# Kernel tuning notes

Measured on AMD Instinct MI355X. Metric: run time of the kernel, lower is better.

## Reference

```python
import jax, jax.numpy as jnp
import numpy as np

N = 50000        # nodes
E = 800000       # edges (avg degree 16)
IN = 256         # in_feature_dim
H = 4            # heads_num
F = 64           # out_feature_dim per head (H*F == IN)
NEG_SLOPE = 0.2  # LeakyReLU slope used for both scoring and output activation


def setup_inputs() -> dict:
    key = jax.random.key(0)
    ks = jax.random.split(key, 8)
    x = jax.random.normal(ks[0], (N, IN), dtype=jnp.float32)
    edge_src = jax.random.randint(ks[1], (E,), 0, N, dtype=jnp.int32)
    edge_trg = jax.random.randint(ks[2], (E,), 0, N, dtype=jnp.int32)
    # xavier-ish scaled params
    W = jax.random.normal(ks[3], (IN, H * F), dtype=jnp.float32) * 0.06
    a_src = jax.random.normal(ks[4], (H, F), dtype=jnp.float32) * 0.1
    a_trg = jax.random.normal(ks[5], (H, F), dtype=jnp.float32) * 0.1
    skip_w = jax.random.normal(ks[6], (IN, H * F), dtype=jnp.float32) * 0.06
    bias = jnp.zeros((H * F,), dtype=jnp.float32)
    return {"x": x, "W": W, "a_src": a_src, "a_trg": a_trg,
            "skip_w": skip_w, "bias": bias,
            "edge_src": edge_src, "edge_trg": edge_trg}


def _leaky(v):
    return jnp.where(v > 0, v, NEG_SLOPE * v)


def reference(x, W, a_src, a_trg, skip_w, bias, edge_src, edge_trg):
    n_nodes = x.shape[0]
    # node-wise projection: [N, H, F]
    proj = (x @ W).reshape(n_nodes, H, F)
    # per-head attention scores: [N, H]
    s_src = jnp.einsum('nhf,hf->nh', proj, a_src)
    s_trg = jnp.einsum('nhf,hf->nh', proj, a_trg)
    # lift to edges + LeakyReLU scoring: [E, H]
    e = _leaky(s_src[edge_src] + s_trg[edge_trg])
    # neighborhood-aware (scatter) softmax over incoming edges of each target
    e = e - jnp.max(e)                      # global max subtraction, as in the source
    ex = jnp.exp(e)
    denom = jax.ops.segment_sum(ex, edge_trg, num_segments=n_nodes)  # [N, H]
    attn = ex / (denom[edge_trg] + 1e-16)   # [E, H]
    # weighted aggregation: [E, H, F] -> scatter-add -> [N, H, F]
    weighted = proj[edge_src] * attn[..., None]
    out = jax.ops.segment_sum(weighted, edge_trg, num_segments=n_nodes)
    # skip connection (dims differ: in=256 vs per-head 64 -> use skip_proj)
    out = out + (x @ skip_w).reshape(n_nodes, H, F)
    # concat heads + bias + output activation (default LeakyReLU 0.2)
    out = out.reshape(n_nodes, H * F) + bias
    return _leaky(out)
```

## Files before the change

### kernel.cpp

```cpp
#include <hip/hip_runtime.h>
#include <math.h>

constexpr float SLOPE = 0.2f;

typedef __bf16 bf16x8 __attribute__((ext_vector_type(8)));
typedef __bf16 bf16x4 __attribute__((ext_vector_type(4)));
typedef float  f32x4  __attribute__((ext_vector_type(4)));

__device__ __forceinline__ int imin(int a, int b) { return a < b ? a : b; }

__device__ __forceinline__ void glds16(const void* g, void* l) {
    __builtin_amdgcn_global_load_lds(
        (const __attribute__((address_space(1))) unsigned int*)g,
        (__attribute__((address_space(3))) unsigned int*)l,
        16, 0, 0);
}

__global__ __launch_bounds__(256) void prep_k(
    const float* __restrict__ W, const float* __restrict__ skw,
    __bf16* __restrict__ Bt,
    const float* __restrict__ x, __bf16* __restrict__ xb, int nxv, int nxb,
    const int* __restrict__ etrg, int* __restrict__ cnt, int E)
{
    const int b = blockIdx.x;
    if (b < 512) {
        const int i = b * 256 + threadIdx.x;
        const int n = i >> 8, k = i & 255;
        const float v = (n < 256) ? W[k * 256 + n] : skw[k * 256 + (n - 256)];
        Bt[i] = (__bf16)v;
    } else if (b < 512 + nxb) {
        const int gid = (b - 512) * 256 + threadIdx.x;
        if (gid < nxv) {
            const float4 f0 = *(const float4*)(x + (size_t)gid * 8);
            const float4 f1 = *(const float4*)(x + (size_t)gid * 8 + 4);
            bf16x8 v;
            v[0] = (__bf16)f0.x; v[1] = (__bf16)f0.y;
            v[2] = (__bf16)f0.z; v[3] = (__bf16)f0.w;
            v[4] = (__bf16)f1.x; v[5] = (__bf16)f1.y;
            v[6] = (__bf16)f1.z; v[7] = (__bf16)f1.w;
            *(bf16x8*)(xb + (size_t)gid * 8) = v;
        }
    } else {
        const int e = (b - 512 - nxb) * 256 + threadIdx.x;
        if (e < E) atomicAdd(&cnt[etrg[e]], 1);
    }
}

__global__ __launch_bounds__(256, 2) void gemm_mfma(
    const __bf16* __restrict__ xb, const __bf16* __restrict__ Bt,
    __bf16* __restrict__ projb, float* __restrict__ out, int M)
{
    __shared__ __bf16 As[256 * 32];
    __shared__ __bf16 Bs[128 * 32];

    const int t    = threadIdx.x;
    const int w    = t >> 6;
    const int lane = t & 63;
    const int q    = lane >> 4;
    const int ln   = lane & 15;

    const int row0 = blockIdx.x * 256;
    const int bt0  = blockIdx.y * 128;

    f32x4 acc[4][8] = {};

    for (int k0 = 0; k0 < 256; k0 += 32) {
#pragma unroll
        for (int p = 0; p < 4; ++p) {
            const int idx = p * 256 + t;
            const int r   = idx >> 2;
            const int ko  = (idx & 3) * 8;
            const int ga  = imin(row0 + r, M - 1);
            glds16(xb + (size_t)ga * 256 + k0 + ko, &As[idx * 8]);
        }
#pragma unroll
        for (int p = 0; p < 2; ++p) {
            const int idx = p * 256 + t;
            const int r   = idx >> 2;
            const int ko  = (idx & 3) * 8;
            glds16(Bt + (size_t)(bt0 + r) * 256 + k0 + ko, &Bs[idx * 8]);
        }
        asm volatile("s_waitcnt vmcnt(0)" ::: "memory");
        __syncthreads();

        bf16x8 af[4], bfr[8];
#pragma unroll
        for (int rb = 0; rb < 4; ++rb)
            af[rb] = *(const bf16x8*)&As[(w * 64 + rb * 16 + ln) * 32 + q * 8];
#pragma unroll
        for (int cb = 0; cb < 8; ++cb)
            bfr[cb] = *(const bf16x8*)&Bs[(cb * 16 + ln) * 32 + q * 8];
#pragma unroll
        for (int rb = 0; rb < 4; ++rb)
#pragma unroll
            for (int cb = 0; cb < 8; ++cb)
                acc[rb][cb] = __builtin_amdgcn_mfma_f32_16x16x32_bf16(
                    af[rb], bfr[cb], acc[rb][cb], 0, 0, 0);
        __syncthreads();
    }

    const bool isProj  = (blockIdx.y < 2);
    const int  colbase = (blockIdx.y & 1) * 128;
#pragma unroll
    for (int rb = 0; rb < 4; ++rb) {
#pragma unroll
        for (int r = 0; r < 4; ++r) {
            const int grow = row0 + w * 64 + rb * 16 + q * 4 + r;
            if (grow < M) {
#pragma unroll
                for (int cb = 0; cb < 8; ++cb) {
                    const float v = acc[rb][cb][r];
                    const int gcol = colbase + cb * 16 + ln;
                    if (isProj) projb[(size_t)grow * 256 + gcol] = (__bf16)v;
                    else        out[(size_t)grow * 256 + gcol]   = v;
                }
            }
        }
    }
}

__global__ __launch_bounds__(256) void scores_k(
    const __bf16* __restrict__ projb,
    const float* __restrict__ a_src, const float* __restrict__ a_trg,
    float* __restrict__ s_src, float* __restrict__ s_trg, int N)
{
    const int nid  = blockIdx.x * 4 + (threadIdx.x >> 6);
    const int lane = threadIdx.x & 63;
    if (nid >= N) return;

    const bf16x4 p4  = *(const bf16x4*)(projb + (size_t)nid * 256 + lane * 4);
    const float4 as4 = *(const float4*)(a_src + lane * 4);
    const float4 at4 = *(const float4*)(a_trg + lane * 4);

    float vs = (float)p4[0] * as4.x + (float)p4[1] * as4.y +
               (float)p4[2] * as4.z + (float)p4[3] * as4.w;
    float vt = (float)p4[0] * at4.x + (float)p4[1] * at4.y +
               (float)p4[2] * at4.z + (float)p4[3] * at4.w;

#pragma unroll
    for (int d = 8; d > 0; d >>= 1) {
        vs += __shfl_down(vs, d, 16);
        vt += __shfl_down(vt, d, 16);
    }
    if ((lane & 15) == 0) {
        s_src[nid * 4 + (lane >> 4)] = vs;
        s_trg[nid * 4 + (lane >> 4)] = vt;
    }
}

__global__ __launch_bounds__(1024) void scanA(
    const int* __restrict__ cnt, int* __restrict__ off, int* __restrict__ bsum, int N)
{
    __shared__ int wsum[16];
    const int t = threadIdx.x;
    const int lane = t & 63;
    const int w = t >> 6;
    const int i = blockIdx.x * 1024 + t;
    const int v = (i < N) ? cnt[i] : 0;

    int s = v;
#pragma unroll
    for (int d = 1; d < 64; d <<= 1) {
        int o = __shfl_up(s, d);
        if (lane >= d) s += o;
    }
    if (lane == 63) wsum[w] = s;
    __syncthreads();
    if (w == 0 && lane < 16) {
        int ws = wsum[lane];
        int sc = ws;
#pragma unroll
        for (int d = 1; d < 16; d <<= 1) {
            int o = __shfl_up(sc, d);
            if (lane >= d) sc += o;
        }
        wsum[lane] = sc - ws;
    }
    __syncthreads();
    const int excl = wsum[w] + s - v;
    if (i < N) off[i] = excl;
    if (t == 1023) bsum[blockIdx.x] = excl + v;
}

__global__ __launch_bounds__(256) void scanBC(
    int* __restrict__ off, const int* __restrict__ bsum, int* __restrict__ cur,
    int N, int E)
{
    const int i = blockIdx.x * 256 + threadIdx.x;
    const int chunk = blockIdx.x >> 2;
    const int lane = threadIdx.x & 63;

    int v = (lane < chunk) ? bsum[lane] : 0;
#pragma unroll
    for (int d = 1; d < 64; d <<= 1) v += __shfl_xor(v, d);

    if (i < N) {
        const int o = off[i] + v;
        off[i] = o;
        cur[i] = o;
    }
    if (i == 0) off[N] = E;
}

__global__ __launch_bounds__(256) void scatter_k(
    const int* __restrict__ esrc, const int* __restrict__ etrg,
    int* __restrict__ cur, int* __restrict__ srcs, int E)
{
    const int e = blockIdx.x * 256 + threadIdx.x;
    if (e < E) {
        const int pos = atomicAdd(&cur[etrg[e]], 1);
        srcs[pos] = esrc[e];
    }
}

__global__ __launch_bounds__(256) void aggregate_wave(
    const int* __restrict__ off, const int* __restrict__ srcs,
    const float* __restrict__ s_src, const float* __restrict__ s_trg,
    const __bf16* __restrict__ projb, const float* __restrict__ bias,
    float* __restrict__ out, int N)
{
    const int w = threadIdx.x >> 6;
    const int l = threadIdx.x & 63;
    const int n = blockIdx.x * 4 + w;
    if (n >= N) return;

    const int h  = l >> 4;
    const int je = l & 7;
    const float st = s_trg[n * 4 + h];
    const int b0 = off[n], b1 = off[n + 1];

    f32x4 acc = {0.f, 0.f, 0.f, 0.f};
    float denom = 0.f;

    int i = b0;
    for (; i + 8 <= b1; i += 8) {
        const int s0 = srcs[i + je];
        float v = s_src[s0 * 4 + h] + st;
        v = v > 0.f ? v : SLOPE * v;
        const float ex = __expf(v);

        int s[8];
#pragma unroll
        for (int j = 0; j < 8; ++j) s[j] = __shfl(s0, j);

        bf16x4 p[8];
#pragma unroll
        for (int j = 0; j < 8; ++j)
            p[j] = *(const bf16x4*)(projb + (size_t)((unsigned)s[j] * 256u) + l * 4);

        float e[8];
#pragma unroll
        for (int j = 0; j < 8; ++j) e[j] = __shfl(ex, (l & 48) | j);

#pragma unroll
        for (int j = 0; j < 8; ++j) {
            denom += e[j];
            acc[0] += e[j] * (float)p[j][0];
            acc[1] += e[j] * (float)p[j][1];
            acc[2] += e[j] * (float)p[j][2];
            acc[3] += e[j] * (float)p[j][3];
        }
    }
    for (; i < b1; ++i) {
        const int s = srcs[i];
        float v = s_src[s * 4 + h] + st;
        v = v > 0.f ? v : SLOPE * v;
        const float ex = __expf(v);
        denom += ex;
        const bf16x4 p = *(const bf16x4*)(projb + (size_t)((unsigned)s * 256u) + l * 4);
        acc[0] += ex * (float)p[0];
        acc[1] += ex * (float)p[1];
        acc[2] += ex * (float)p[2];
        acc[3] += ex * (float)p[3];
    }

    const size_t o = (size_t)n * 256 + l * 4;
    const float4 sk = *(const float4*)(out + o);
    const float4 b4 = *(const float4*)(bias + l * 4);
    const float inv = 1.f / (denom + 1e-16f);
    float4 r;
    r.x = acc[0] * inv + sk.x + b4.x;
    r.y = acc[1] * inv + sk.y + b4.y;
    r.z = acc[2] * inv + sk.z + b4.z;
    r.w = acc[3] * inv + sk.w + b4.w;
    r.x = r.x > 0.f ? r.x : SLOPE * r.x;
    r.y = r.y > 0.f ? r.y : SLOPE * r.y;
    r.z = r.z > 0.f ? r.z : SLOPE * r.z;
    r.w = r.w > 0.f ? r.w : SLOPE * r.w;
    *(float4*)(out + o) = r;
}

extern "C" void kernel_launch(void* const* d_in, const int* in_sizes, int n_in,
                              void* d_out, int out_size, void* d_ws, size_t ws_size,
                              hipStream_t stream)
{
    const float* x     = (const float*)d_in[0];
    const float* W     = (const float*)d_in[1];
    const float* a_src = (const float*)d_in[2];
    const float* a_trg = (const float*)d_in[3];
    const float* skw   = (const float*)d_in[4];
    const float* bias  = (const float*)d_in[5];
    const int*   esrc  = (const int*)d_in[6];
    const int*   etrg  = (const int*)d_in[7];

    const int N = in_sizes[0] / 256;
    const int E = in_sizes[6];
    float* out = (float*)d_out;

    __bf16* projb = (__bf16*)d_ws;
    __bf16* Bt    = projb + (size_t)N * 256;
    __bf16* xb    = Bt + 512 * 256;
    float*  s_src = (float*)(xb + (size_t)N * 256);
    float*  s_trg = s_src + (size_t)N * 4;
    int*    cnt   = (int*)(s_trg + (size_t)N * 4);
    int*    off   = cnt + N;
    int*    cur   = off + (N + 1);
    int*    bsum  = cur + N;
    int*    srcs  = bsum + 64;

    const int nxv = (N * 256) / 8;
    const int nxb = (nxv + 255) / 256;
    const int nhb = (E + 255) / 256;
    const int nsc = (N + 1023) / 1024;

    hipMemsetAsync(cnt, 0, (size_t)N * sizeof(int), stream);

    prep_k<<<512 + nxb + nhb, 256, 0, stream>>>(W, skw, Bt, x, xb, nxv, nxb,
                                                etrg, cnt, E);

    dim3 g((N + 255) / 256, 4);
    gemm_mfma<<<g, 256, 0, stream>>>(xb, Bt, projb, out, N);

    scores_k<<<(N + 3) / 4, 256, 0, stream>>>(projb, a_src, a_trg, s_src, s_trg, N);

    scanA<<<nsc, 1024, 0, stream>>>(cnt, off, bsum, N);
    scanBC<<<(N + 255) / 256, 256, 0, stream>>>(off, bsum, cur, N, E);

    scatter_k<<<(E + 255) / 256, 256, 0, stream>>>(esrc, etrg, cur, srcs, E);

    aggregate_wave<<<(N + 3) / 4, 256, 0, stream>>>(off, srcs, s_src, s_trg,
                                                    projb, bias, out, N);
}
```

Baseline: 311.7 us.

## Split wave into two half-waves gathering 16-byte rows over 16-edge batches

Restructures the per-node aggregation so each half of the wave handles alternate edges, with every lane loading 8 bf16 features (16 bytes) instead of 4. Each iteration now covers 16 edges, and a masked tail replaces the scalar remainder loop. The two halves' partial sums and denominators are combined with a cross-half shuffle before the epilogue. The aim is wider, fewer gather loads and more memory parallelism per wave, at the cost of more accumulator registers and some extra shuffles and reduction work.

```diff
diff --git a/kernel.cpp b/kernel.cpp
--- a/kernel.cpp
+++ b/kernel.cpp
@@ -224,65 +224,85 @@
     const int n = blockIdx.x * 4 + w;
     if (n >= N) return;
 
-    const int h  = l >> 4;
-    const int je = l & 7;
-    const float st = s_trg[n * 4 + h];
+    const int jj   = l & 15;
+    const int hh   = l >> 4;
+    const int half = l >> 5;
+    const int ll   = l & 31;
+    const int h    = ll >> 3;
+
+    const float st = s_trg[n * 4 + hh];
     const int b0 = off[n], b1 = off[n + 1];
 
-    f32x4 acc = {0.f, 0.f, 0.f, 0.f};
+    float acc[8] = {};
     float denom = 0.f;
 
     int i = b0;
-    for (; i + 8 <= b1; i += 8) {
-        const int s0 = srcs[i + je];
-        float v = s_src[s0 * 4 + h] + st;
+    for (; i + 16 <= b1; i += 16) {
+        const int s_mine = srcs[i + jj];
+        float v = s_src[s_mine * 4 + hh] + st;
         v = v > 0.f ? v : SLOPE * v;
         const float ex = __expf(v);
 
-        int s[8];
-#pragma unroll
-        for (int j = 0; j < 8; ++j) s[j] = __shfl(s0, j);
-
-        bf16x4 p[8];
-#pragma unroll
-        for (int j = 0; j < 8; ++j)
-            p[j] = *(const bf16x4*)(projb + (size_t)((unsigned)s[j] * 256u) + l * 4);
+        int sj[8];
+#pragma unroll
+        for (int t = 0; t < 8; ++t) sj[t] = __shfl(s_mine, 2 * t + half);
+
+        bf16x8 p[8];
+#pragma unroll
+        for (int t = 0; t < 8; ++t)
+            p[t] = *(const bf16x8*)(projb + (size_t)((unsigned)sj[t] * 256u) + ll * 8);
 
         float e[8];
 #pragma unroll
-        for (int j = 0; j < 8; ++j) e[j] = __shfl(ex, (l & 48) | j);
-
-#pragma unroll
-        for (int j = 0; j < 8; ++j) {
-            denom += e[j];
-            acc[0] += e[j] * (float)p[j][0];
-            acc[1] += e[j] * (float)p[j][1];
-            acc[2] += e[j] * (float)p[j][2];
-            acc[3] += e[j] * (float)p[j][3];
-        }
-    }
-    for (; i < b1; ++i) {
-        const int s = srcs[i];
-        float v = s_src[s * 4 + h] + st;
+        for (int t = 0; t < 8; ++t) e[t] = __shfl(ex, (h << 4) | (2 * t + half));
+
+#pragma unroll
+        for (int t = 0; t < 8; ++t) {
+            denom += e[t];
+#pragma unroll
+            for (int k = 0; k < 8; ++k)
+                acc[k] += e[t] * (float)p[t][k];
+        }
+    }
+
+    const int rem = b1 - i;
+    if (rem > 0) {
+        const int s_mine = srcs[i + (jj < rem ? jj : rem - 1)];
+        float v = s_src[s_mine * 4 + hh] + st;
         v = v > 0.f ? v : SLOPE * v;
-        const float ex = __expf(v);
-        denom += ex;
-        const bf16x4 p = *(const bf16x4*)(projb + (size_t)((unsigned)s * 256u) + l * 4);
-        acc[0] += ex * (float)p[0];
-        acc[1] += ex * (float)p[1];
-        acc[2] += ex * (float)p[2];
-        acc[3] += ex * (float)p[3];
-    }
-
-    const size_t o = (size_t)n * 256 + l * 4;
+        const float ex = (jj < rem) ? __expf(v) : 0.f;
+
+#pragma unroll
+        for (int t = 0; t < 8; ++t) {
+            const int j2 = 2 * t + half;
+            const int   sj = __shfl(s_mine, j2);
+            const float e  = __shfl(ex, (h << 4) | j2);
+            if (j2 < rem) {
+                const bf16x8 p =
+                    *(const bf16x8*)(projb + (size_t)((unsigned)sj * 256u) + ll * 8);
+                denom += e;
+#pragma unroll
+                for (int k = 0; k < 8; ++k)
+                    acc[k] += e * (float)p[k];
+            }
+        }
+    }
+
+#pragma unroll
+    for (int k = 0; k < 8; ++k) acc[k] += __shfl_xor(acc[k], 32);
+    denom += __shfl_xor(denom, 32);
+
+    const int    kb    = half * 4;
+    const int    fbase = ll * 8 + kb;
+    const size_t o     = (size_t)n * 256 + fbase;
     const float4 sk = *(const float4*)(out + o);
-    const float4 b4 = *(const float4*)(bias + l * 4);
+    const float4 b4 = *(const float4*)(bias + fbase);
     const float inv = 1.f / (denom + 1e-16f);
     float4 r;
-    r.x = acc[0] * inv + sk.x + b4.x;
-    r.y = acc[1] * inv + sk.y + b4.y;
-    r.z = acc[2] * inv + sk.z + b4.z;
-    r.w = acc[3] * inv + sk.w + b4.w;
+    r.x = acc[kb + 0] * inv + sk.x + b4.x;
+    r.y = acc[kb + 1] * inv + sk.y + b4.y;
+    r.z = acc[kb + 2] * inv + sk.z + b4.z;
+    r.w = acc[kb + 3] * inv + sk.w + b4.w;
     r.x = r.x > 0.f ? r.x : SLOPE * r.x;
     r.y = r.y > 0.f ? r.y : SLOPE * r.y;
     r.z = r.z > 0.f ? r.z : SLOPE * r.z;
```

After: 310.5 us. Within noise of the previous version (-0.4%).
